# Performance work log

Hardware: AMD Instinct MI355X
Metric: run time of the kernel (lower is better)

## Reference

```python
import jax, jax.numpy as jnp
import numpy as np

B, S, HIDDEN, H, HD = 4, 1024, 1024, 16, 64  # head_dim = hidden/heads; rel-pos 'd_model' = HD
TABLE = 2 * HD - 1  # 127


def setup_inputs() -> dict:
    key = jax.random.key(0)
    ks = jax.random.split(key, 16)
    sc = 0.02
    return {
        "query": jax.random.normal(ks[0], (B, S, HIDDEN), jnp.float32),
        "key": jax.random.normal(ks[1], (B, S, HIDDEN), jnp.float32),
        "value": jax.random.normal(ks[2], (B, S, HIDDEN), jnp.float32),
        "Wq": jax.random.normal(ks[3], (H, HIDDEN, HD), jnp.float32) * sc,
        "Wk": jax.random.normal(ks[4], (H, HIDDEN, HD), jnp.float32) * sc,
        "Wv": jax.random.normal(ks[5], (H, HIDDEN, HD), jnp.float32) * sc,
        "bq": jax.random.normal(ks[6], (H, HD), jnp.float32) * sc,
        "bk": jax.random.normal(ks[7], (H, HD), jnp.float32) * sc,
        "bv": jax.random.normal(ks[8], (H, HD), jnp.float32) * sc,
        "rp_k_table": jax.random.normal(ks[9], (TABLE, HD), jnp.float32) * sc,
        "rp_v_table": jax.random.normal(ks[10], (TABLE, HD), jnp.float32) * sc,
        "Wfc": jax.random.normal(ks[11], (HIDDEN, HIDDEN), jnp.float32) * sc,
        "bfc": jax.random.normal(ks[12], (HIDDEN,), jnp.float32) * sc,
    }


def _rel_bias(table, length, hd):
    # distance clipped to [-(hd-1), hd-1], shifted -> index into (2*hd-1, hd) table
    i = jnp.arange(length)
    idx = jnp.clip(i[None, :] - i[:, None], -(hd - 1), hd - 1) + (hd - 1)
    return table[idx]  # [S, S, hd]


def reference(query, key, value, Wq, Wk, Wv, bq, bk, bv, rp_k_table, rp_v_table, Wfc, bfc):
    hd = Wq.shape[-1]
    b, s, _ = query.shape
    k_bias = _rel_bias(rp_k_table, s, hd)  # [S,S,hd], shared across heads
    v_bias = _rel_bias(rp_v_table, s, hd)
    # per-head projections: [B,H,S,hd]
    q = jnp.einsum('bsh,nhd->bnsd', query, Wq) + bq[None, :, None, :]
    kk = jnp.einsum('bsh,nhd->bnsd', key, Wk) + bk[None, :, None, :]
    v = jnp.einsum('bsh,nhd->bnsd', value, Wv) + bv[None, :, None, :]
    # scores: QK^T plus Shaw-style relative-position key bias
    scores = (jnp.einsum('bnid,bnjd->bnij', q, kk)
              + jnp.einsum('bnid,ijd->bnij', q, k_bias)) / (hd ** 0.5)
    w = jax.nn.softmax(scores, axis=-1)  # [B,H,S,S]
    out = (jnp.einsum('bnij,bnjd->bnid', w, v)
           + jnp.einsum('bnij,ijd->bnid', w, v_bias))  # [B,H,S,hd]
    hidden = out.transpose(0, 2, 1, 3).reshape(b, s, -1)  # concat heads
    return hidden @ Wfc.T + bfc
```

## Files before the change

kernel.cpp:

```cpp
#include <hip/hip_runtime.h>
#include <stdint.h>

typedef unsigned int u32;
typedef unsigned short u16;
typedef float f32x4 __attribute__((ext_vector_type(4)));
typedef __bf16 bfx8 __attribute__((ext_vector_type(8)));
typedef short s16x8 __attribute__((ext_vector_type(8)));
typedef short s16x4 __attribute__((ext_vector_type(4)));
typedef int i32x4 __attribute__((ext_vector_type(4)));

#define DEVI static __device__ __forceinline__

#if __has_builtin(__builtin_amdgcn_exp2f)
#define EXP2(x) __builtin_amdgcn_exp2f(x)
#else
#define EXP2(x) exp2f(x)
#endif


DEVI u16 f2bf(float f){
  u32 u = __builtin_bit_cast(u32, f);
  u32 r = (u + 0x7fffu + ((u >> 16) & 1u)) >> 16;
  return (u16)r;
}
DEVI float b2f(u16 v){ return __builtin_bit_cast(float, (u32)v << 16); }

DEVI f32x4 mfma16(s16x8 a, s16x8 b, f32x4 c){
  return __builtin_amdgcn_mfma_f32_16x16x32_bf16(
      __builtin_bit_cast(bfx8, a), __builtin_bit_cast(bfx8, b), c, 0, 0, 0);
}

DEVI void gld16(const void* g, void* l){
  __builtin_amdgcn_global_load_lds(
      (__attribute__((address_space(1))) void*)g,
      (__attribute__((address_space(3))) void*)l, 16, 0, 0);
}

__global__ void cast3_kernel(const float* __restrict__ a, const float* __restrict__ b,
                             const float* __restrict__ c, u16* __restrict__ dst){
  const long n_each = 4194304;
  long stride = (long)gridDim.x * blockDim.x;
  for (long v = (long)blockIdx.x * blockDim.x + threadIdx.x; v < 3 * n_each / 8; v += stride){
    long idx8 = v * 8;
    int which = (int)(idx8 / n_each);
    long off = idx8 - (long)which * n_each;
    const float* s = which == 0 ? a : (which == 1 ? b : c);
    float4 f0 = *(const float4*)(s + off);
    float4 f1 = *(const float4*)(s + off + 4);
    s16x8 o;
    o[0]=(short)f2bf(f0.x); o[1]=(short)f2bf(f0.y); o[2]=(short)f2bf(f0.z); o[3]=(short)f2bf(f0.w);
    o[4]=(short)f2bf(f1.x); o[5]=(short)f2bf(f1.y); o[6]=(short)f2bf(f1.z); o[7]=(short)f2bf(f1.w);
    *(s16x8*)(dst + idx8) = o;
  }
}

__global__ void cast1_kernel(const float* __restrict__ a, u16* __restrict__ dst, long n){
  long stride = (long)gridDim.x * blockDim.x;
  for (long v = (long)blockIdx.x * blockDim.x + threadIdx.x; v < n / 8; v += stride){
    long idx8 = v * 8;
    float4 f0 = *(const float4*)(a + idx8);
    float4 f1 = *(const float4*)(a + idx8 + 4);
    s16x8 o;
    o[0]=(short)f2bf(f0.x); o[1]=(short)f2bf(f0.y); o[2]=(short)f2bf(f0.z); o[3]=(short)f2bf(f0.w);
    o[4]=(short)f2bf(f1.x); o[5]=(short)f2bf(f1.y); o[6]=(short)f2bf(f1.z); o[7]=(short)f2bf(f1.w);
    *(s16x8*)(dst + idx8) = o;
  }
}

__global__ void wtrans_kernel(const float* __restrict__ Wq, const float* __restrict__ Wk,
                              const float* __restrict__ Wv, u16* __restrict__ Wt){
  int bid = blockIdx.x;
  int kt = bid & 15; int h = (bid >> 4) & 15; int proj = bid >> 8;
  const float* W = (proj == 0 ? Wq : (proj == 1 ? Wk : Wv)) + (long)h * (1024 * 64);
  __shared__ u16 lt[64][66];
  int t = threadIdx.x;
  #pragma unroll
  for (int it = 0; it < 16; ++it){
    int idx = it * 256 + t;
    int r = idx >> 6, d = idx & 63;
    lt[r][d] = f2bf(W[(long)(kt * 64 + r) * 64 + d]);
  }
  __syncthreads();
  long outbase = (long)proj * 1024 + h * 64;
  #pragma unroll
  for (int it = 0; it < 16; ++it){
    int idx = it * 256 + t;
    int d = idx >> 6, r = idx & 63;
    Wt[(outbase + d) * 1024 + kt * 64 + r] = lt[r][d];
  }
}

__global__ void tables_kernel(const float* __restrict__ rpk, const float* __restrict__ rpv,
                              u16* __restrict__ rpkb, u16* __restrict__ rpvT){
  int t = threadIdx.x;
  for (int i = t; i < 128 * 64; i += 256){
    int row = i >> 6, d = i & 63;
    rpkb[i] = (row < 127) ? f2bf(rpk[row * 64 + d]) : (u16)0;
  }
  for (int i = t; i < 64 * 128; i += 256){
    int d = i >> 7, row = i & 127;
    rpvT[i] = (row < 127) ? f2bf(rpv[row * 64 + d]) : (u16)0;
  }
}

__global__ void vtrans_kernel(const u16* __restrict__ Vb, u16* __restrict__ Vt){
  int bid = blockIdx.x;
  int st = bid & 15, bh = bid >> 4;
  const u16* src = Vb + ((long)bh * 1024 + st * 64) * 64;
  u16* dst = Vt + (long)bh * 64 * 1024 + st * 64;
  __shared__ u16 lt[64][66];
  int t = threadIdx.x;
  #pragma unroll
  for (int it = 0; it < 16; ++it){
    int idx = it * 256 + t;
    int r = idx >> 6, d = idx & 63;
    lt[r][d] = src[idx];
  }
  __syncthreads();
  #pragma unroll
  for (int it = 0; it < 16; ++it){
    int idx = it * 256 + t;
    int d = idx >> 6, r = idx & 63;
    dst[(long)d * 1024 + r] = lt[r][d];
  }
}

DEVI void gemm_core(const u16* __restrict__ A, const u16* __restrict__ Bt,
                    int m0, int n0, u16* lds, int tid, f32x4 (&acc)[4][4]){
  const int K = 1024;
  int w = tid >> 6, lane = tid & 63, g = lane >> 4, li = lane & 15;
  int wm = w >> 1, wn = w & 1;
  for (int ks = 0; ks < 16; ++ks){
    int k0 = ks * 64;
    __syncthreads();
    #pragma unroll
    for (int i = 0; i < 4; ++i){
      int c = i * 256 + w * 64 + lane;
      int r = c >> 3, s = lane & 7;
      int kk = k0 + ((s ^ (r & 7)) << 3);
      gld16(A + (long)(m0 + r) * K + kk, (char*)lds + (i * 256 + w * 64) * 16);
      gld16(Bt + (long)(n0 + r) * K + kk, (char*)lds + 16384 + (i * 256 + w * 64) * 16);
    }
    __syncthreads();
    #pragma unroll
    for (int kh = 0; kh < 2; ++kh){
      s16x8 af[4], bfr[4];
      #pragma unroll
      for (int mi = 0; mi < 4; ++mi){
        int row = wm * 64 + mi * 16 + li;
        int byt = (row * 128 + (kh * 32 + g * 8) * 2) ^ ((li & 7) << 4);
        af[mi] = *(const s16x8*)((const char*)lds + byt);
      }
      #pragma unroll
      for (int ni = 0; ni < 4; ++ni){
        int row = wn * 64 + ni * 16 + li;
        int byt = 16384 + ((row * 128 + (kh * 32 + g * 8) * 2) ^ ((li & 7) << 4));
        bfr[ni] = *(const s16x8*)((const char*)lds + byt);
      }
      #pragma unroll
      for (int mi = 0; mi < 4; ++mi)
        #pragma unroll
        for (int ni = 0; ni < 4; ++ni)
          acc[mi][ni] = mfma16(af[mi], bfr[ni], acc[mi][ni]);
    }
  }
}

__launch_bounds__(256, 2)
__global__ void gemm_qkv(const u16* __restrict__ Xb, const u16* __restrict__ Wt,
                         const float* __restrict__ bq, const float* __restrict__ bk,
                         const float* __restrict__ bv,
                         u16* __restrict__ Qb, u16* __restrict__ Kb, u16* __restrict__ Vb){
  __shared__ __align__(16) u16 lds[16384];
  int tid = threadIdx.x;
  int bo = blockIdx.x;
  int bidx = (bo & 7) * 96 + (bo >> 3);
  int bn = bidx % 24, bm = bidx / 24;
  int m0 = bm * 128, n0 = bn * 128;
  int proj = n0 >> 10;
  const u16* A = Xb + (long)proj * 4096 * 1024;
  f32x4 acc[4][4] = {};
  gemm_core(A, Wt, m0, n0, lds, tid, acc);
  int w = tid >> 6, lane = tid & 63, g = lane >> 4, li = lane & 15;
  int wm = w >> 1, wn = w & 1;
  const float* bias = proj == 0 ? bq : (proj == 1 ? bk : bv);
  u16* Dst = proj == 0 ? Qb : (proj == 1 ? Kb : Vb);
  float scale = (proj == 0) ? 0.125f * 1.44269504f : 1.0f;
  #pragma unroll
  for (int mi = 0; mi < 4; ++mi)
    #pragma unroll
    for (int ni = 0; ni < 4; ++ni)
      #pragma unroll
      for (int r = 0; r < 4; ++r){
        int m = m0 + wm * 64 + mi * 16 + g * 4 + r;
        int n = n0 + wn * 64 + ni * 16 + li;
        int nn = n & 1023;
        float v = (acc[mi][ni][r] + bias[nn]) * scale;
        int b = m >> 10, s = m & 1023;
        int h = nn >> 6, d = nn & 63;
        Dst[((long)(b * 16 + h) * 1024 + s) * 64 + d] = f2bf(v);
      }
}

__launch_bounds__(256, 2)
__global__ void gemm_fc(const u16* __restrict__ Hid, const u16* __restrict__ Wfcb,
                        const float* __restrict__ bfc, float* __restrict__ out){
  __shared__ __align__(16) u16 lds[16384];
  int tid = threadIdx.x;
  int bidx = blockIdx.x;
  int bn = bidx & 7, bm = bidx >> 3;
  int m0 = bm * 128, n0 = bn * 128;
  f32x4 acc[4][4] = {};
  gemm_core(Hid, Wfcb, m0, n0, lds, tid, acc);
  int w = tid >> 6, lane = tid & 63, g = lane >> 4, li = lane & 15;
  int wm = w >> 1, wn = w & 1;
  #pragma unroll
  for (int mi = 0; mi < 4; ++mi)
    #pragma unroll
    for (int ni = 0; ni < 4; ++ni)
      #pragma unroll
      for (int r = 0; r < 4; ++r){
        int m = m0 + wm * 64 + mi * 16 + g * 4 + r;
        int n = n0 + wn * 64 + ni * 16 + li;
        out[(long)m * 1024 + n] = acc[mi][ni][r] + bfc[n];
      }
}

__launch_bounds__(256, 2)
__global__ void attn_kernel(const u16* __restrict__ Qb, const u16* __restrict__ Kb,
                            const u16* __restrict__ Vt, const u16* __restrict__ rpkb,
                            const u16* __restrict__ rpvT, u16* __restrict__ Hid){
  const int S = 1024;
  int bh = blockIdx.y;
  int i0 = blockIdx.x * 64;
  int bb = bh >> 4, hh = bh & 15;
  const u16* Qp = Qb + (long)bh * S * 64;
  const u16* Kp = Kb + (long)bh * S * 64;
  const u16* Vp = Vt + (long)bh * 64 * S;
  int tid = threadIdx.x, w = tid >> 6, lane = tid & 63, g = lane >> 4, li = lane & 15;

  __shared__ __align__(16) char smem[35840];
  u16* rqb  = (u16*)smem;
  u16* bw   = (u16*)(smem + 16384);
  float* redL = (float*)(smem + 32768);
  float* redR = redL + 256;
  float* redD = redR + 256;
  float* Ored = (float*)smem;

  s16x8 qf[4][2];
  #pragma unroll
  for (int ni = 0; ni < 4; ++ni)
    #pragma unroll
    for (int kh = 0; kh < 2; ++kh)
      qf[ni][kh] = *(const s16x8*)(Qp + (long)(i0 + ni * 16 + li) * 64 + kh * 32 + g * 8);

  {
    i32x4 z = {0, 0, 0, 0};
    #pragma unroll
    for (int i = 0; i < 4; ++i) ((i32x4*)bw)[i * 256 + tid] = z;
  }

  #pragma unroll
  for (int tt = 0; tt < 2; ++tt){
    int tb = w * 2 + tt;
    s16x8 pf0 = *(const s16x8*)(rpkb + (tb * 16 + li) * 64 + g * 8);
    s16x8 pf1 = *(const s16x8*)(rpkb + (tb * 16 + li) * 64 + 32 + g * 8);
    #pragma unroll
    for (int ni = 0; ni < 4; ++ni){
      f32x4 r = {0.f, 0.f, 0.f, 0.f};
      r = mfma16(qf[ni][0], pf0, r);
      r = mfma16(qf[ni][1], pf1, r);
      #pragma unroll
      for (int e = 0; e < 4; ++e)
        rqb[(ni * 16 + g * 4 + e) * 128 + tb * 16 + li] = f2bf(r[e]);
    }
  }
  __syncthreads();

  float rqL[4], rqR[4];
  #pragma unroll
  for (int ni = 0; ni < 4; ++ni){
    int iloc = ni * 16 + li;
    rqL[ni] = b2f(rqb[iloc * 128]);
    rqR[ni] = b2f(rqb[iloc * 128 + 126]);
  }

  f32x4 oacc[4][4] = {};
  float dacc[4] = {0, 0, 0, 0}, Lac[4] = {0, 0, 0, 0}, Rac[4] = {0, 0, 0, 0};

  for (int jt = 0; jt < 8; ++jt){
    int jw = jt * 128 + w * 32;
    s16x8 kf[2][2];
    #pragma unroll
    for (int mi = 0; mi < 2; ++mi)
      #pragma unroll
      for (int kh = 0; kh < 2; ++kh)
        kf[mi][kh] = *(const s16x8*)(Kp + (long)(jw + mi * 16 + li) * 64 + kh * 32 + g * 8);
    s16x8 av[4];
    #pragma unroll
    for (int mi = 0; mi < 2; ++mi){
      int js0 = jw + mi * 16;
      f32x4 sacc[4];
      #pragma unroll
      for (int ni = 0; ni < 4; ++ni){
        f32x4 s0 = {0.f, 0.f, 0.f, 0.f};
        s0 = mfma16(kf[mi][0], qf[ni][0], s0);
        s0 = mfma16(kf[mi][1], qf[ni][1], s0);
        sacc[ni] = s0;
      }
      if (js0 >= i0 + 126){
        #pragma unroll
        for (int ni = 0; ni < 4; ++ni)
          #pragma unroll
          for (int r = 0; r < 4; ++r){
            float e = EXP2(sacc[ni][r] + rqR[ni]);
            dacc[ni] += e; Rac[ni] += e;
            av[ni][mi * 4 + r] = (short)f2bf(e);
          }
      } else if (js0 + 78 <= i0){
        #pragma unroll
        for (int ni = 0; ni < 4; ++ni)
          #pragma unroll
          for (int r = 0; r < 4; ++r){
            float e = EXP2(sacc[ni][r] + rqL[ni]);
            dacc[ni] += e; Lac[ni] += e;
            av[ni][mi * 4 + r] = (short)f2bf(e);
          }
      } else {
        #pragma unroll
        for (int ni = 0; ni < 4; ++ni){
          int iloc = ni * 16 + li;
          #pragma unroll
          for (int r = 0; r < 4; ++r){
            int jgl = js0 + g * 4 + r;
            int delta = jgl - (i0 + iloc);
            int dcl = delta < -62 ? -62 : (delta > 62 ? 62 : delta);
            int tg = dcl + 63;
            float rqv = b2f(rqb[iloc * 128 + tg]);
            bool lft = delta < -62, rgt = delta > 62;
            rqv = lft ? rqL[ni] : (rgt ? rqR[ni] : rqv);
            float e = EXP2(sacc[ni][r] + rqv);
            dacc[ni] += e;
            u16 eb = f2bf(e);
            av[ni][mi * 4 + r] = (short)eb;
            if (!lft && !rgt){
              int byt = (iloc * 256 + tg * 2) ^ ((iloc & 7) << 4);
              *(u16*)((char*)bw + byt) = eb;
            }
            Lac[ni] += lft ? e : 0.f;
            Rac[ni] += rgt ? e : 0.f;
          }
        }
      }
    }
    #pragma unroll
    for (int nd = 0; nd < 4; ++nd){
      const u16* vp = Vp + (long)(nd * 16 + li) * S + jw + g * 4;
      s16x4 vlo = *(const s16x4*)(vp);
      s16x4 vhi = *(const s16x4*)(vp + 16);
      s16x8 vv;
      vv[0]=vlo[0]; vv[1]=vlo[1]; vv[2]=vlo[2]; vv[3]=vlo[3];
      vv[4]=vhi[0]; vv[5]=vhi[1]; vv[6]=vhi[2]; vv[7]=vhi[3];
      #pragma unroll
      for (int ni = 0; ni < 4; ++ni)
        oacc[ni][nd] = mfma16(av[ni], vv, oacc[ni][nd]);
    }
  }

  #pragma unroll
  for (int ni = 0; ni < 4; ++ni){
    dacc[ni] += __shfl_xor(dacc[ni], 16); dacc[ni] += __shfl_xor(dacc[ni], 32);
    Lac[ni]  += __shfl_xor(Lac[ni], 16);  Lac[ni]  += __shfl_xor(Lac[ni], 32);
    Rac[ni]  += __shfl_xor(Rac[ni], 16);  Rac[ni]  += __shfl_xor(Rac[ni], 32);
  }
  if (g == 0){
    #pragma unroll
    for (int ni = 0; ni < 4; ++ni){
      redL[w * 64 + ni * 16 + li] = Lac[ni];
      redR[w * 64 + ni * 16 + li] = Rac[ni];
      redD[w * 64 + ni * 16 + li] = dacc[ni];
    }
  }
  __syncthreads();
  if (tid < 64){
    int i = tid;
    float Ls = redL[i] + redL[64 + i] + redL[128 + i] + redL[192 + i];
    float Rs = redR[i] + redR[64 + i] + redR[128 + i] + redR[192 + i];
    float Ds = redD[i] + redD[64 + i] + redD[128 + i] + redD[192 + i];
    *(u16*)((char*)bw + ((i * 256 + 0)   ^ ((i & 7) << 4))) = f2bf(Ls);
    *(u16*)((char*)bw + ((i * 256 + 252) ^ ((i & 7) << 4))) = f2bf(Rs);
    redD[i] = Ds;
  }
  for (int ww = 0; ww < 4; ++ww){
    if (w == ww){
      #pragma unroll
      for (int ni = 0; ni < 4; ++ni)
        #pragma unroll
        for (int nd = 0; nd < 4; ++nd)
          #pragma unroll
          for (int r = 0; r < 4; ++r){
            int i = ni * 16 + g * 4 + r, d = nd * 16 + li;
            if (ww == 0) Ored[i * 64 + d] = oacc[ni][nd][r];
            else         Ored[i * 64 + d] += oacc[ni][nd][r];
          }
    }
    __syncthreads();
  }
  s16x8 rvf[4];
  #pragma unroll
  for (int ksl = 0; ksl < 4; ++ksl)
    rvf[ksl] = *(const s16x8*)(rpvT + (w * 16 + li) * 128 + ksl * 32 + g * 8);
  f32x4 bacc[4];
  #pragma unroll
  for (int mi = 0; mi < 4; ++mi){
    f32x4 a4 = {0.f, 0.f, 0.f, 0.f};
    #pragma unroll
    for (int ksl = 0; ksl < 4; ++ksl){
      int row = mi * 16 + li;
      int byt = (row * 256 + (ksl * 32 + g * 8) * 2) ^ ((row & 7) << 4);
      s16x8 a = *(const s16x8*)((const char*)bw + byt);
      a4 = mfma16(a, rvf[ksl], a4);
    }
    bacc[mi] = a4;
  }
  #pragma unroll
  for (int mi = 0; mi < 4; ++mi)
    #pragma unroll
    for (int r = 0; r < 4; ++r){
      int i = mi * 16 + g * 4 + r;
      float den = redD[i];
      float o = (Ored[i * 64 + w * 16 + li] + bacc[mi][r]) / den;
      Hid[((long)bb * S + i0 + i) * 1024 + hh * 64 + w * 16 + li] = f2bf(o);
    }
}

extern "C" void kernel_launch(void* const* d_in, const int* in_sizes, int n_in,
                              void* d_out, int out_size, void* d_ws, size_t ws_size,
                              hipStream_t stream){
  const float* query = (const float*)d_in[0];
  const float* key   = (const float*)d_in[1];
  const float* value = (const float*)d_in[2];
  const float* Wq  = (const float*)d_in[3];
  const float* Wk  = (const float*)d_in[4];
  const float* Wv  = (const float*)d_in[5];
  const float* bq  = (const float*)d_in[6];
  const float* bk  = (const float*)d_in[7];
  const float* bv  = (const float*)d_in[8];
  const float* rpk = (const float*)d_in[9];
  const float* rpv = (const float*)d_in[10];
  const float* Wfc = (const float*)d_in[11];
  const float* bfc = (const float*)d_in[12];
  float* out = (float*)d_out;

  u16* Xb   = (u16*)d_ws;
  u16* Wt   = Xb + 3L * 4096 * 1024;
  u16* Wfcb = Wt + 3072L * 1024;
  u16* rpkb = Wfcb + 1024L * 1024;
  u16* rpvT = rpkb + 128 * 64;
  u16* Qb   = rpvT + 64 * 128;
  u16* Kb   = Qb + 64L * 1024 * 64;
  u16* Vb   = Kb + 64L * 1024 * 64;
  u16* Vt   = Vb + 64L * 1024 * 64;
  u16* Hid  = Vt + 64L * 1024 * 64;

  cast3_kernel<<<2048, 256, 0, stream>>>(query, key, value, Xb);
  cast1_kernel<<<512, 256, 0, stream>>>(Wfc, Wfcb, 1024L * 1024);
  wtrans_kernel<<<768, 256, 0, stream>>>(Wq, Wk, Wv, Wt);
  tables_kernel<<<1, 256, 0, stream>>>(rpk, rpv, rpkb, rpvT);
  gemm_qkv<<<768, 256, 0, stream>>>(Xb, Wt, bq, bk, bv, Qb, Kb, Vb);
  vtrans_kernel<<<1024, 256, 0, stream>>>(Vb, Vt);
  attn_kernel<<<dim3(16, 64), 256, 0, stream>>>(Qb, Kb, Vt, rpkb, rpvT, Hid);
  gemm_fc<<<256, 256, 0, stream>>>(Hid, Wfcb, bfc, out);
}
```

Measured before the change: 272.2 us.

## Double-buffer K/V register loads across tiles and trim softmax accumulations

Restructures the attention tile loop so the K and V fragments for the next tile load into a second register buffer while the current tile computes, hiding global-load latency behind MFMA and exp work. The float-to-bf16 conversion now uses the compiler's native bf16 cast instead of manual rounding. The row-sum accumulator is updated only for in-band elements, and the left and right sums are added back once at the reduction step. The prefetch raises register pressure and, on the last iteration, reads one tile past the end of the K/V rows without using the values.

New measurement: 263.9 us. -3.0%, faster.

```diff
diff --git a/kernel.cpp b/kernel.cpp
--- a/kernel.cpp
+++ b/kernel.cpp
@@ -24,6 +24,10 @@
   return (u16)r;
 }
 DEVI float b2f(u16 v){ return __builtin_bit_cast(float, (u32)v << 16); }
+DEVI short e2s(float f){ return __builtin_bit_cast(short, (__bf16)f); }
+
+struct s16x4p { s16x4 lo, hi; };
+DEVI s16x8 cat4(s16x4 lo, s16x4 hi){ s16x4p p{lo, hi}; return __builtin_bit_cast(s16x8, p); }
 
 DEVI f32x4 mfma16(s16x8 a, s16x8 b, f32x4 c){
   return __builtin_amdgcn_mfma_f32_16x16x32_bf16(
@@ -288,14 +292,26 @@
   f32x4 oacc[4][4] = {};
   float dacc[4] = {0, 0, 0, 0}, Lac[4] = {0, 0, 0, 0}, Rac[4] = {0, 0, 0, 0};
 
-  for (int jt = 0; jt < 8; ++jt){
+  auto LOADKV = [&](int jt, s16x8 (&kf)[2][2], s16x8 (&vv)[4]){
     int jw = jt * 128 + w * 32;
-    s16x8 kf[2][2];
     #pragma unroll
     for (int mi = 0; mi < 2; ++mi)
       #pragma unroll
       for (int kh = 0; kh < 2; ++kh)
         kf[mi][kh] = *(const s16x8*)(Kp + (long)(jw + mi * 16 + li) * 64 + kh * 32 + g * 8);
+    #pragma unroll
+    for (int nd = 0; nd < 4; ++nd){
+      const u16* vp = Vp + (long)(nd * 16 + li) * S + jw + g * 4;
+      s16x4 vlo = *(const s16x4*)(vp);
+      s16x4 vhi = *(const s16x4*)(vp + 16);
+      vv[nd] = cat4(vlo, vhi);
+    }
+  };
+
+  auto BODY = [&](int jt, s16x8 (&kf)[2][2], s16x8 (&vv)[4],
+                  s16x8 (&kfn)[2][2], s16x8 (&vvn)[4]){
+    LOADKV(jt + 1, kfn, vvn);
+    int jw = jt * 128 + w * 32;
     s16x8 av[4];
     #pragma unroll
     for (int mi = 0; mi < 2; ++mi){
@@ -314,8 +330,8 @@
           #pragma unroll
           for (int r = 0; r < 4; ++r){
             float e = EXP2(sacc[ni][r] + rqR[ni]);
-            dacc[ni] += e; Rac[ni] += e;
-            av[ni][mi * 4 + r] = (short)f2bf(e);
+            Rac[ni] += e;
+            av[ni][mi * 4 + r] = e2s(e);
           }
       } else if (js0 + 78 <= i0){
         #pragma unroll
@@ -323,8 +339,8 @@
           #pragma unroll
           for (int r = 0; r < 4; ++r){
             float e = EXP2(sacc[ni][r] + rqL[ni]);
-            dacc[ni] += e; Lac[ni] += e;
-            av[ni][mi * 4 + r] = (short)f2bf(e);
+            Lac[ni] += e;
+            av[ni][mi * 4 + r] = e2s(e);
           }
       } else {
         #pragma unroll
@@ -340,12 +356,12 @@
             bool lft = delta < -62, rgt = delta > 62;
             rqv = lft ? rqL[ni] : (rgt ? rqR[ni] : rqv);
             float e = EXP2(sacc[ni][r] + rqv);
-            dacc[ni] += e;
-            u16 eb = f2bf(e);
-            av[ni][mi * 4 + r] = (short)eb;
+            short eb = e2s(e);
+            av[ni][mi * 4 + r] = eb;
             if (!lft && !rgt){
               int byt = (iloc * 256 + tg * 2) ^ ((iloc & 7) << 4);
-              *(u16*)((char*)bw + byt) = eb;
+              *(u16*)((char*)bw + byt) = (u16)eb;
+              dacc[ni] += e;
             }
             Lac[ni] += lft ? e : 0.f;
             Rac[ni] += rgt ? e : 0.f;
@@ -354,17 +370,17 @@
       }
     }
     #pragma unroll
-    for (int nd = 0; nd < 4; ++nd){
-      const u16* vp = Vp + (long)(nd * 16 + li) * S + jw + g * 4;
-      s16x4 vlo = *(const s16x4*)(vp);
-      s16x4 vhi = *(const s16x4*)(vp + 16);
-      s16x8 vv;
-      vv[0]=vlo[0]; vv[1]=vlo[1]; vv[2]=vlo[2]; vv[3]=vlo[3];
-      vv[4]=vhi[0]; vv[5]=vhi[1]; vv[6]=vhi[2]; vv[7]=vhi[3];
+    for (int nd = 0; nd < 4; ++nd)
       #pragma unroll
       for (int ni = 0; ni < 4; ++ni)
-        oacc[ni][nd] = mfma16(av[ni], vv, oacc[ni][nd]);
-    }
+        oacc[ni][nd] = mfma16(av[ni], vv[nd], oacc[ni][nd]);
+  };
+
+  s16x8 kfA[2][2], kfB[2][2], vvA[4], vvB[4];
+  LOADKV(0, kfA, vvA);
+  for (int jtp = 0; jtp < 4; ++jtp){
+    BODY(2 * jtp,     kfA, vvA, kfB, vvB);
+    BODY(2 * jtp + 1, kfB, vvB, kfA, vvA);
   }
 
   #pragma unroll
@@ -386,7 +402,7 @@
     int i = tid;
     float Ls = redL[i] + redL[64 + i] + redL[128 + i] + redL[192 + i];
     float Rs = redR[i] + redR[64 + i] + redR[128 + i] + redR[192 + i];
-    float Ds = redD[i] + redD[64 + i] + redD[128 + i] + redD[192 + i];
+    float Ds = redD[i] + redD[64 + i] + redD[128 + i] + redD[192 + i] + Ls + Rs;
     *(u16*)((char*)bw + ((i * 256 + 0)   ^ ((i & 7) << 4))) = f2bf(Ls);
     *(u16*)((char*)bw + ((i * 256 + 252) ^ ((i & 7) << 4))) = f2bf(Rs);
     redD[i] = Ds;
```
